# Kernel tuning notes

Hardware: AMD Instinct MI355X
Metric: run time of the kernel (lower is better)

Reference implementation:

```python
import jax, jax.numpy as jnp
import numpy as np

B, D, H, E, K, A = 65536, 44, 256, 4, 2, 8  # batch, state_dim, hidden, experts, top_k, action_dim


def setup_inputs() -> dict:
    key = jax.random.key(0)
    ks = jax.random.split(key, 10)
    s = 0.1  # weight scale
    return dict(
        state=jax.random.normal(ks[0], (B, D), dtype=jnp.float32),
        rW1=jax.random.normal(ks[1], (D, H // 2)) * s, rb1=jnp.zeros((H // 2,)),
        rW2=jax.random.normal(ks[2], (H // 2, E)) * s, rb2=jnp.zeros((E,)),
        eW1=jax.random.normal(ks[3], (E, D, H)) * s, eb1=jnp.zeros((E, H)),
        eg1=jnp.ones((E, H)), ebt1=jnp.zeros((E, H)),
        eW2=jax.random.normal(ks[4], (E, H, H)) * s, eb2=jnp.zeros((E, H)),
        eg2=jnp.ones((E, H)), ebt2=jnp.zeros((E, H)),
        eW3=jax.random.normal(ks[5], (E, H, 2 * A)) * s, eb3=jnp.zeros((E, 2 * A)),
        vW1=jax.random.normal(ks[6], (D, H)) * s, vb1=jnp.zeros((H,)),
        vg=jnp.ones((H,)), vbt=jnp.zeros((H,)),
        vW2=jax.random.normal(ks[7], (H, H // 2)) * s, vb2=jnp.zeros((H // 2,)),
        vW3=jax.random.normal(ks[8], (H // 2, 1)) * s, vb3=jnp.zeros((1,)),
    )


def _ln(x, g, b):
    m = jnp.mean(x, axis=-1, keepdims=True)
    v = jnp.mean(jnp.square(x - m), axis=-1, keepdims=True)
    return (x - m) * jax.lax.rsqrt(v + 1e-5) * g + b


def reference(state, rW1, rb1, rW2, rb2,
              eW1, eb1, eg1, ebt1, eW2, eb2, eg2, ebt2, eW3, eb3,
              vW1, vb1, vg, vbt, vW2, vb2, vW3, vb3):
    # Router (eval mode: no noise)
    h = jax.nn.relu(state @ rW1 + rb1)
    router_probs = jax.nn.softmax(h @ rW2 + rb2, axis=-1)          # [B, E]
    top_v, top_i = jax.lax.top_k(router_probs, K)                  # [B, K]
    top_v = top_v / (jnp.sum(top_v, axis=-1, keepdims=True) + 1e-8)
    # Dense combine weights per expert (equivalent to per-sample gather/scatter loop)
    combine = jnp.sum(jax.nn.one_hot(top_i, E, dtype=state.dtype) * top_v[..., None], axis=1)  # [B, E]

    def expert(W1, b1, g1, bt1, W2, b2, g2, bt2, W3, b3):
        y = jax.nn.relu(_ln(state @ W1 + b1, g1, bt1))   # [B, H]
        y = jax.nn.relu(_ln(y @ W2 + b2, g2, bt2))       # [B, H]
        return y @ W3 + b3                               # [B, 2A]

    eout = jax.vmap(expert)(eW1, eb1, eg1, ebt1, eW2, eb2, eg2, ebt2, eW3, eb3)  # [E, B, 2A]
    mix = jnp.einsum('ebd,be->bd', eout, combine)        # [B, 2A]

    alpha = jax.nn.softplus(mix[:, :A]) + 1.0
    beta = jax.nn.softplus(mix[:, A:]) + 1.0

    v = jax.nn.relu(_ln(state @ vW1 + vb1, vg, vbt))
    v = jax.nn.relu(v @ vW2 + vb2)
    value = v @ vW3 + vb3                                # [B, 1]
    return alpha, beta, value, router_probs
```

## Files before the change

### kernel.cpp

```cpp
#include <hip/hip_runtime.h>
#include <math.h>

#define NB 65536

using f32x4 = __attribute__((ext_vector_type(4))) float;
using u32x4 = __attribute__((ext_vector_type(4))) unsigned;
using bf16x8 = __attribute__((ext_vector_type(8))) __bf16;

__device__ __forceinline__ unsigned pk2(float lo, float hi) {
    return (unsigned)__builtin_bit_cast(unsigned short, (__bf16)lo)
         | ((unsigned)__builtin_bit_cast(unsigned short, (__bf16)hi) << 16);
}
__device__ __forceinline__ float softplus_f(float x) {
    return fmaxf(x, 0.f) + log1pf(expf(-fabsf(x)));
}

#define MFMA16(acc, a, b) acc = __builtin_amdgcn_mfma_f32_16x16x32_bf16(a, b, acc, 0, 0, 0)

__device__ __forceinline__ bf16x8 cvt8(f32x4 a, f32x4 b) {
    union { bf16x8 v; unsigned u[4]; } r;
    r.u[0] = pk2(a[0], a[1]); r.u[1] = pk2(a[2], a[3]);
    r.u[2] = pk2(b[0], b[1]); r.u[3] = pk2(b[2], b[3]);
    return r.v;
}

__device__ __forceinline__ const bf16x8* ys_frag(const unsigned short* ys, int row, int col) {
    return (const bf16x8*)&ys[row * 256 + (col ^ ((row & 7) << 3))];
}

template<int NJ>
__device__ __forceinline__ void ldch(f32x4* r, const f32x4* __restrict__ src, int tid) {
    #pragma unroll
    for (int j = 0; j < NJ; ++j) r[j] = src[tid + j * 256];
}
template<int NJ>
__device__ __forceinline__ void wrch(unsigned short* buf, const f32x4* r, int tid) {
    #pragma unroll
    for (int j = 0; j < NJ; ++j) *(f32x4*)&buf[(size_t)(tid + j * 256) * 8] = r[j];
}

template<int NT>
__device__ __forceinline__ void mfma_bcols(f32x4* acc, bf16x8 a, const unsigned short* bufp, int c, int g) {
    #pragma unroll
    for (int t = 0; t < NT; ++t) {
        bf16x8 b = *(const bf16x8*)&bufp[t * 512 + g * 128 + c * 8];
        MFMA16(acc[t], a, b);
    }
}

__device__ __forceinline__ void ln_relu_store(
    f32x4* acc, const float* bs, const float* gs, const float* ts,
    unsigned int* ysu, int stripe, int g, int c)
{
    #pragma unroll
    for (int t = 0; t < 16; ++t) {
        float bb = bs[t * 16 + c];
        #pragma unroll
        for (int r = 0; r < 4; ++r) acc[t][r] += bb;
    }
    float sum[4] = {0.f, 0.f, 0.f, 0.f}, sq[4] = {0.f, 0.f, 0.f, 0.f};
    #pragma unroll
    for (int t = 0; t < 16; ++t) {
        #pragma unroll
        for (int r = 0; r < 4; ++r) { sum[r] += acc[t][r]; sq[r] += acc[t][r] * acc[t][r]; }
    }
    #pragma unroll
    for (int m = 1; m < 16; m <<= 1) {
        #pragma unroll
        for (int r = 0; r < 4; ++r) { sum[r] += __shfl_xor(sum[r], m); sq[r] += __shfl_xor(sq[r], m); }
    }
    float rs[4], nm[4];
    #pragma unroll
    for (int r = 0; r < 4; ++r) {
        float mean = sum[r] * (1.f / 256.f);
        float var = sq[r] * (1.f / 256.f) - mean * mean;
        rs[r] = rsqrtf(var + 1e-5f);
        nm[r] = -mean * rs[r];
    }
    const int odd = c & 1;
    const int ra = stripe + g * 4 + (odd ? 2 : 0);
    const int sza = (ra & 7) << 2, szb = ((ra + 1) & 7) << 2;
    #pragma unroll
    for (int t = 0; t < 16; ++t) {
        float gg = gs[t * 16 + c], bb = ts[t * 16 + c];
        float v0 = fmaxf(fmaf(fmaf(acc[t][0], rs[0], nm[0]), gg, bb), 0.f);
        float v1 = fmaxf(fmaf(fmaf(acc[t][1], rs[1], nm[1]), gg, bb), 0.f);
        float v2 = fmaxf(fmaf(fmaf(acc[t][2], rs[2], nm[2]), gg, bb), 0.f);
        float v3 = fmaxf(fmaf(fmaf(acc[t][3], rs[3], nm[3]), gg, bb), 0.f);
        float o0 = __shfl_xor(v0, 1), o1 = __shfl_xor(v1, 1);
        float o2 = __shfl_xor(v2, 1), o3 = __shfl_xor(v3, 1);
        unsigned p0 = pk2(odd ? o0 : v0, odd ? v0 : o0);
        unsigned p1 = pk2(odd ? o1 : v1, odd ? v1 : o1);
        unsigned p2 = pk2(odd ? o2 : v2, odd ? v2 : o2);
        unsigned p3 = pk2(odd ? o3 : v3, odd ? v3 : o3);
        unsigned pa = odd ? p2 : p0;
        unsigned pb = odd ? p3 : p1;
        int cp = t * 8 + (c >> 1);
        ysu[ra * 128 + (cp ^ sza)] = pa;
        ysu[(ra + 1) * 128 + (cp ^ szb)] = pb;
    }
}

__global__ __launch_bounds__(256) void k1_prep_router(
    const float* __restrict__ state,
    const float* __restrict__ rW1, const float* __restrict__ rb1,
    const float* __restrict__ rW2, const float* __restrict__ rb2,
    const float* __restrict__ eW1, const float* __restrict__ eW2, const float* __restrict__ eW3,
    const float* __restrict__ vW1, const float* __restrict__ vW2,
    unsigned int* __restrict__ w1img, unsigned int* __restrict__ w2img,
    unsigned int* __restrict__ vw1img, unsigned int* __restrict__ vw2img,
    unsigned int* __restrict__ w3img,
    float* __restrict__ out_probs, float* __restrict__ combine)
{
    __shared__ f32x4 pl[256];
    const int blk = blockIdx.x;
    if (blk < 192) {
        int fid = blk * 256 + threadIdx.x;
        float v[8];
        unsigned int* dst;
        if (fid < 8192) {
            int e = fid >> 11, ch = (fid >> 10) & 1, rr = fid & 1023;
            int t = rr >> 6, g = (rr >> 4) & 3, c = rr & 15;
            int h = t * 16 + c, k0 = ch * 32 + g * 8;
            #pragma unroll
            for (int j = 0; j < 8; ++j) {
                int k = k0 + j;
                v[j] = (k < 44) ? eW1[(e * 44 + k) * 256 + h] : 0.f;
            }
            dst = w1img + (size_t)fid * 4;
        } else if (fid < 40960) {
            int f = fid - 8192;
            int e = f >> 13, ch = (f >> 10) & 7, rr = f & 1023;
            int t = rr >> 6, g = (rr >> 4) & 3, c = rr & 15;
            int h = t * 16 + c, k0 = ch * 32 + g * 8;
            const float* base = eW2 + (size_t)e * 65536 + h;
            #pragma unroll
            for (int j = 0; j < 8; ++j) v[j] = base[(size_t)(k0 + j) * 256];
            dst = w2img + (size_t)f * 4;
        } else if (fid < 43008) {
            int f = fid - 40960;
            int ch = f >> 10, rr = f & 1023;
            int t = rr >> 6, g = (rr >> 4) & 3, c = rr & 15;
            int h = t * 16 + c, k0 = ch * 32 + g * 8;
            #pragma unroll
            for (int j = 0; j < 8; ++j) {
                int k = k0 + j;
                v[j] = (k < 44) ? vW1[k * 256 + h] : 0.f;
            }
            dst = vw1img + (size_t)f * 4;
        } else if (fid < 47104) {
            int f = fid - 43008;
            int ch = f >> 9, rr = f & 511;
            int t = rr >> 6, g = (rr >> 4) & 3, c = rr & 15;
            int h = t * 16 + c, k0 = ch * 32 + g * 8;
            #pragma unroll
            for (int j = 0; j < 8; ++j) v[j] = vW2[(k0 + j) * 128 + h];
            dst = vw2img + (size_t)f * 4;
        } else {
            int f = fid - 47104;
            int e = f >> 9, rr = f & 511;
            int s = rr >> 6, g = (rr >> 4) & 3, o = rr & 15;
            int k0 = s * 32 + g * 8;
            #pragma unroll
            for (int j = 0; j < 8; ++j) v[j] = eW3[(size_t)e * 4096 + (k0 + j) * 16 + o];
            dst = w3img + (size_t)f * 4;
        }
        u32x4 out;
        #pragma unroll
        for (int p = 0; p < 4; ++p) out[p] = pk2(v[2 * p], v[2 * p + 1]);
        *(u32x4*)dst = out;
        return;
    }

    const int tid = threadIdx.x;
    const int wid = tid >> 6;
    const int lane = tid & 63;
    const int brow = (blk - 192) * 64;
    const int w32 = __builtin_amdgcn_readfirstlane(wid * 32);

    {
        float s[44];
        const float* srow = state + (size_t)(brow + lane) * 44;
        #pragma unroll
        for (int d4 = 0; d4 < 11; ++d4) {
            f32x4 v = *(const f32x4*)(srow + d4 * 4);
            s[d4 * 4 + 0] = v[0]; s[d4 * 4 + 1] = v[1];
            s[d4 * 4 + 2] = v[2]; s[d4 * 4 + 3] = v[3];
        }
        const float* w1b = rW1 + w32;
        f32x4 h[8];
        #pragma unroll
        for (int j = 0; j < 8; ++j) h[j] = *(const f32x4*)&rb1[w32 + j * 4];
        #pragma unroll
        for (int d = 0; d < 44; ++d) {
            #pragma unroll
            for (int j = 0; j < 8; ++j)
                h[j] += s[d] * *(const f32x4*)(w1b + d * 128 + j * 4);
        }
        f32x4 l = {0.f, 0.f, 0.f, 0.f};
        #pragma unroll
        for (int j = 0; j < 8; ++j) {
            #pragma unroll
            for (int cmp = 0; cmp < 4; ++cmp) {
                float hv = fmaxf(h[j][cmp], 0.f);
                l += hv * *(const f32x4*)&rW2[(w32 + j * 4 + cmp) * 4];
            }
        }
        pl[wid * 64 + lane] = l;
    }
    __syncthreads();
    if (wid == 0) {
        f32x4 lg = pl[lane] + pl[64 + lane] + pl[128 + lane] + pl[192 + lane];
        lg += *(const f32x4*)rb2;
        float l0 = lg[0], l1 = lg[1], l2 = lg[2], l3 = lg[3];
        float mx = fmaxf(fmaxf(l0, l1), fmaxf(l2, l3));
        float e0 = expf(l0 - mx), e1 = expf(l1 - mx), e2 = expf(l2 - mx), e3 = expf(l3 - mx);
        float inv = 1.f / (e0 + e1 + e2 + e3);
        float p0 = e0 * inv, p1 = e1 * inv, p2 = e2 * inv, p3 = e3 * inv;
        f32x4 probs = {p0, p1, p2, p3};
        *(f32x4*)&out_probs[(size_t)(brow + lane) * 4] = probs;

        int i1 = 0; float v1 = p0;
        if (p1 > v1) { v1 = p1; i1 = 1; }
        if (p2 > v1) { v1 = p2; i1 = 2; }
        if (p3 > v1) { v1 = p3; i1 = 3; }
        int i2 = -1; float v2 = -1.f;
        if (i1 != 0 && p0 > v2) { v2 = p0; i2 = 0; }
        if (i1 != 1 && p1 > v2) { v2 = p1; i2 = 1; }
        if (i1 != 2 && p2 > v2) { v2 = p2; i2 = 2; }
        if (i1 != 3 && p3 > v2) { v2 = p3; i2 = 3; }
        float cn = 1.f / (v1 + v2 + 1e-8f);
        float c1 = v1 * cn, c2 = v2 * cn;
        f32x4 cm;
        cm[0] = (i1 == 0) ? c1 : (i2 == 0) ? c2 : 0.f;
        cm[1] = (i1 == 1) ? c1 : (i2 == 1) ? c2 : 0.f;
        cm[2] = (i1 == 2) ? c1 : (i2 == 2) ? c2 : 0.f;
        cm[3] = (i1 == 3) ? c1 : (i2 == 3) ? c2 : 0.f;
        *(f32x4*)&combine[(size_t)(brow + lane) * 4] = cm;
    }
}

#define SM_YS    0
#define SM_BUFA  32768
#define SM_BUFB  49152
#define SM_B1    65536
#define SM_G1    66560
#define SM_T1    67584
#define SM_B2    68608
#define SM_G2    69632
#define SM_T2    70656
#define SM_B3    71680
#define SM_CMB   71744
#define SM_TOTAL 72768

#define SWAPBUF() { unsigned short* _t = cur; cur = nxt; nxt = _t; }

__global__ __launch_bounds__(256, 2) void k2_experts_value(
    const float* __restrict__ state,
    const float* __restrict__ eb1, const float* __restrict__ eg1, const float* __restrict__ ebt1,
    const float* __restrict__ eb2, const float* __restrict__ eg2, const float* __restrict__ ebt2,
    const float* __restrict__ eb3,
    const float* __restrict__ vb1, const float* __restrict__ vg, const float* __restrict__ vbt,
    const float* __restrict__ vb2, const float* __restrict__ vW3, const float* __restrict__ vb3,
    const f32x4* __restrict__ w1v, const f32x4* __restrict__ w2v,
    const f32x4* __restrict__ vw1v, const f32x4* __restrict__ vw2v,
    const f32x4* __restrict__ w3v,
    const float* __restrict__ combine,
    float* __restrict__ out_alpha, float* __restrict__ out_beta, float* __restrict__ out_value)
{
    __shared__ __align__(16) unsigned char smem[SM_TOTAL];
    unsigned short* ys = (unsigned short*)(smem + SM_YS);
    unsigned int* ysu = (unsigned int*)(smem + SM_YS);
    float* b1s = (float*)(smem + SM_B1);
    float* g1s = (float*)(smem + SM_G1);
    float* t1s = (float*)(smem + SM_T1);
    float* b2s = (float*)(smem + SM_B2);
    float* g2s = (float*)(smem + SM_G2);
    float* t2s = (float*)(smem + SM_T2);
    float* b3s = (float*)(smem + SM_B3);
    float* cmbs = (float*)(smem + SM_CMB);
    unsigned short* cur = (unsigned short*)(smem + SM_BUFA);
    unsigned short* nxt = (unsigned short*)(smem + SM_BUFB);

    const int tid = threadIdx.x;
    const int wid = tid >> 6;
    const int lane = tid & 63;
    const int c = lane & 15;
    const int g = lane >> 4;
    const int stripe = wid * 16;
    const bool is_expert = (blockIdx.x < 1024);
    const int brow = (is_expert ? blockIdx.x : (blockIdx.x - 1024)) * 64;

    bf16x8 a1[2];
    {
        const float* srow = state + (size_t)(brow + stripe + c) * 44;
        f32x4 v0 = *(const f32x4*)(srow + g * 8);
        f32x4 v1 = *(const f32x4*)(srow + g * 8 + 4);
        a1[0] = cvt8(v0, v1);
        f32x4 z = {0.f, 0.f, 0.f, 0.f};
        f32x4 w0 = z, w1 = z;
        if (g == 0) { w0 = *(const f32x4*)(srow + 32); w1 = *(const f32x4*)(srow + 36); }
        else if (g == 1) { w0 = *(const f32x4*)(srow + 40); }
        a1[1] = cvt8(w0, w1);
    }

    f32x4 r[4];

    if (is_expert) {
        cmbs[tid] = combine[(size_t)brow * 4 + tid];
        float mix0 = 0.f, mix1 = 0.f, mix2 = 0.f, mix3 = 0.f;

        ldch<4>(r, w1v, tid);
        wrch<4>(cur, r, tid);
        ldch<4>(r, w1v + 1024, tid);
        __syncthreads();

        for (int e = 0; e < 4; ++e) {
            const int en = (e < 3) ? e + 1 : 3;
            float xb1 = eb1[e * 256 + tid], xg1 = eg1[e * 256 + tid], xt1 = ebt1[e * 256 + tid];
            float xb2 = eb2[e * 256 + tid], xg2 = eg2[e * 256 + tid], xt2 = ebt2[e * 256 + tid];
            b1s[tid] = xb1; g1s[tid] = xg1; t1s[tid] = xt1;
            b2s[tid] = xb2; g2s[tid] = xg2; t2s[tid] = xt2;
            if (tid < 16) b3s[tid] = eb3[e * 16 + tid];

            f32x4 acc1[16];
            #pragma unroll
            for (int t = 0; t < 16; ++t) acc1[t] = (f32x4){0.f, 0.f, 0.f, 0.f};

            wrch<4>(nxt, r, tid);
            ldch<4>(r, w2v + (size_t)(e * 8 + 0) * 1024, tid);
            mfma_bcols<16>(acc1, a1[0], cur, c, g);
            __syncthreads(); SWAPBUF();

            wrch<4>(nxt, r, tid);
            ldch<4>(r, w2v + (size_t)(e * 8 + 1) * 1024, tid);
            mfma_bcols<16>(acc1, a1[1], cur, c, g);
            ln_relu_store(acc1, b1s, g1s, t1s, ysu, stripe, g, c);
            __syncthreads(); SWAPBUF();

            f32x4 acc2[16];
            #pragma unroll
            for (int t = 0; t < 16; ++t) acc2[t] = (f32x4){0.f, 0.f, 0.f, 0.f};

            #pragma unroll
            for (int ch = 0; ch < 7; ++ch) {
                wrch<4>(nxt, r, tid);
                if (ch < 6) ldch<4>(r, w2v + (size_t)(e * 8 + ch + 2) * 1024, tid);
                else        ldch<2>(r, w3v + (size_t)e * 512, tid);
                bf16x8 a = *ys_frag(ys, stripe + c, ch * 32 + g * 8);
                mfma_bcols<16>(acc2, a, cur, c, g);
                __syncthreads(); SWAPBUF();
            }

            wrch<2>(nxt, r, tid);
            ldch<4>(r, w1v + (size_t)(en * 2) * 1024, tid);
            {
                bf16x8 a = *ys_frag(ys, stripe + c, 7 * 32 + g * 8);
                mfma_bcols<16>(acc2, a, cur, c, g);
            }
            ln_relu_store(acc2, b2s, g2s, t2s, ysu, stripe, g, c);
            __syncthreads(); SWAPBUF();

            wrch<4>(nxt, r, tid);
            ldch<4>(r, w1v + (size_t)(en * 2 + 1) * 1024, tid);
            f32x4 acc3 = (f32x4){0.f, 0.f, 0.f, 0.f};
            #pragma unroll
            for (int s = 0; s < 8; ++s) {
                bf16x8 a = *ys_frag(ys, stripe + c, s * 32 + g * 8);
                bf16x8 b = *(const bf16x8*)&cur[s * 512 + g * 128 + c * 8];
                MFMA16(acc3, a, b);
            }
            float bb3 = b3s[c];
            mix0 += cmbs[(stripe + g * 4 + 0) * 4 + e] * (acc3[0] + bb3);
            mix1 += cmbs[(stripe + g * 4 + 1) * 4 + e] * (acc3[1] + bb3);
            mix2 += cmbs[(stripe + g * 4 + 2) * 4 + e] * (acc3[2] + bb3);
            mix3 += cmbs[(stripe + g * 4 + 3) * 4 + e] * (acc3[3] + bb3);
            __syncthreads(); SWAPBUF();
        }

        int row0 = brow + stripe + g * 4;
        float sp0 = softplus_f(mix0) + 1.f;
        float sp1 = softplus_f(mix1) + 1.f;
        float sp2 = softplus_f(mix2) + 1.f;
        float sp3 = softplus_f(mix3) + 1.f;
        if (c < 8) {
            out_alpha[(size_t)(row0 + 0) * 8 + c] = sp0;
            out_alpha[(size_t)(row0 + 1) * 8 + c] = sp1;
            out_alpha[(size_t)(row0 + 2) * 8 + c] = sp2;
            out_alpha[(size_t)(row0 + 3) * 8 + c] = sp3;
        } else {
            out_beta[(size_t)(row0 + 0) * 8 + (c - 8)] = sp0;
            out_beta[(size_t)(row0 + 1) * 8 + (c - 8)] = sp1;
            out_beta[(size_t)(row0 + 2) * 8 + (c - 8)] = sp2;
            out_beta[(size_t)(row0 + 3) * 8 + (c - 8)] = sp3;
        }
    } else {
        b1s[tid] = vb1[tid]; g1s[tid] = vg[tid]; t1s[tid] = vbt[tid];
        if (tid < 128) { b2s[tid] = vb2[tid]; g2s[tid] = vW3[tid]; }

        ldch<4>(r, vw1v, tid);
        wrch<4>(cur, r, tid);
        ldch<4>(r, vw1v + 1024, tid);
        __syncthreads();

        f32x4 acc1[16];
        #pragma unroll
        for (int t = 0; t < 16; ++t) acc1[t] = (f32x4){0.f, 0.f, 0.f, 0.f};

        wrch<4>(nxt, r, tid);
        ldch<2>(r, vw2v, tid);
        mfma_bcols<16>(acc1, a1[0], cur, c, g);
        __syncthreads(); SWAPBUF();

        wrch<4>(nxt, r, tid);
        ldch<2>(r, vw2v + 512, tid);
        mfma_bcols<16>(acc1, a1[1], cur, c, g);
        ln_relu_store(acc1, b1s, g1s, t1s, ysu, stripe, g, c);
        __syncthreads(); SWAPBUF();

        f32x4 acc2[8];
        #pragma unroll
        for (int t = 0; t < 8; ++t) acc2[t] = (f32x4){0.f, 0.f, 0.f, 0.f};

        #pragma unroll
        for (int ch = 0; ch < 7; ++ch) {
            wrch<2>(nxt, r, tid);
            if (ch < 6) ldch<2>(r, vw2v + (size_t)(ch + 2) * 512, tid);
            bf16x8 a = *ys_frag(ys, stripe + c, ch * 32 + g * 8);
            mfma_bcols<8>(acc2, a, cur, c, g);
            __syncthreads(); SWAPBUF();
        }
        {
            bf16x8 a = *ys_frag(ys, stripe + c, 7 * 32 + g * 8);
            mfma_bcols<8>(acc2, a, cur, c, g);
        }

        float part[4] = {0.f, 0.f, 0.f, 0.f};
        #pragma unroll
        for (int t = 0; t < 8; ++t) {
            float bb = b2s[t * 16 + c], ww = g2s[t * 16 + c];
            #pragma unroll
            for (int q = 0; q < 4; ++q) part[q] += fmaxf(acc2[t][q] + bb, 0.f) * ww;
        }
        #pragma unroll
        for (int m = 1; m < 16; m <<= 1) {
            #pragma unroll
            for (int q = 0; q < 4; ++q) part[q] += __shfl_xor(part[q], m);
        }
        if (c == 0) {
            float v3 = vb3[0];
            int row = brow + stripe + g * 4;
            out_value[row + 0] = part[0] + v3;
            out_value[row + 1] = part[1] + v3;
            out_value[row + 2] = part[2] + v3;
            out_value[row + 3] = part[3] + v3;
        }
    }
}

extern "C" void kernel_launch(void* const* d_in, const int* in_sizes, int n_in,
                              void* d_out, int out_size, void* d_ws, size_t ws_size,
                              hipStream_t stream)
{
    const float* state = (const float*)d_in[0];
    const float* rW1  = (const float*)d_in[1];
    const float* rb1  = (const float*)d_in[2];
    const float* rW2  = (const float*)d_in[3];
    const float* rb2  = (const float*)d_in[4];
    const float* eW1  = (const float*)d_in[5];
    const float* eb1  = (const float*)d_in[6];
    const float* eg1  = (const float*)d_in[7];
    const float* ebt1 = (const float*)d_in[8];
    const float* eW2  = (const float*)d_in[9];
    const float* eb2  = (const float*)d_in[10];
    const float* eg2  = (const float*)d_in[11];
    const float* ebt2 = (const float*)d_in[12];
    const float* eW3  = (const float*)d_in[13];
    const float* eb3  = (const float*)d_in[14];
    const float* vW1  = (const float*)d_in[15];
    const float* vb1  = (const float*)d_in[16];
    const float* vg   = (const float*)d_in[17];
    const float* vbt  = (const float*)d_in[18];
    const float* vW2  = (const float*)d_in[19];
    const float* vb2  = (const float*)d_in[20];
    const float* vW3  = (const float*)d_in[21];
    const float* vb3  = (const float*)d_in[22];

    float* out = (float*)d_out;
    float* out_alpha = out;
    float* out_beta  = out + (size_t)NB * 8;
    float* out_value = out + (size_t)NB * 16;
    float* out_probs = out + (size_t)NB * 17;

    char* ws = (char*)d_ws;
    float* combine        = (float*)ws;
    unsigned int* w1img   = (unsigned int*)(ws + 0x100000);
    unsigned int* w2img   = (unsigned int*)(ws + 0x120000);
    unsigned int* vw1img  = (unsigned int*)(ws + 0x1A0000);
    unsigned int* vw2img  = (unsigned int*)(ws + 0x1A8000);
    unsigned int* w3img   = (unsigned int*)(ws + 0x1B8000);

    hipLaunchKernelGGL(k1_prep_router, dim3(1216), dim3(256), 0, stream,
                       state, rW1, rb1, rW2, rb2, eW1, eW2, eW3, vW1, vW2,
                       w1img, w2img, vw1img, vw2img, w3img, out_probs, combine);
    hipLaunchKernelGGL(k2_experts_value, dim3(2048), dim3(256), 0, stream,
                       state, eb1, eg1, ebt1, eb2, eg2, ebt2, eb3,
                       vb1, vg, vbt, vb2, vW3, vb3,
                       (const f32x4*)w1img, (const f32x4*)w2img,
                       (const f32x4*)vw1img, (const f32x4*)vw2img,
                       (const f32x4*)w3img,
                       combine, out_alpha, out_beta, out_value);
}
```

Before: 259.2 us.

## Stage router state in LDS with 2 rows per thread; use non-draining barriers

```diff
diff --git a/kernel.cpp b/kernel.cpp
--- a/kernel.cpp
+++ b/kernel.cpp
@@ -13,6 +13,12 @@
 }
 __device__ __forceinline__ float softplus_f(float x) {
     return fmaxf(x, 0.f) + log1pf(expf(-fabsf(x)));
+}
+
+__device__ __forceinline__ void barrier_nodrain() {
+    asm volatile("s_waitcnt lgkmcnt(0)" ::: "memory");
+    __builtin_amdgcn_s_barrier();
+    __builtin_amdgcn_sched_barrier(0);
 }
 
 #define MFMA16(acc, a, b) acc = __builtin_amdgcn_mfma_f32_16x16x32_bf16(a, b, acc, 0, 0, 0)
@@ -112,7 +118,7 @@
     unsigned int* __restrict__ w3img,
     float* __restrict__ out_probs, float* __restrict__ combine)
 {
-    __shared__ f32x4 pl[256];
+    __shared__ __align__(16) float rsm[44 * 128 + 4 * 128 * 4];
     const int blk = blockIdx.x;
     if (blk < 192) {
         int fid = blk * 256 + threadIdx.x;
@@ -175,42 +181,59 @@
     const int tid = threadIdx.x;
     const int wid = tid >> 6;
     const int lane = tid & 63;
-    const int brow = (blk - 192) * 64;
+    const int brow = (blk - 192) * 128;
+    float* s_lds = rsm;
+    f32x4* pl = (f32x4*)(rsm + 44 * 128);
+
+    {
+        int i = tid & 127, half = tid >> 7;
+        const float* srow = state + (size_t)(brow + i) * 44;
+        int d40 = half ? 6 : 0, d41 = half ? 11 : 6;
+        for (int d4 = d40; d4 < d41; ++d4) {
+            f32x4 v = *(const f32x4*)(srow + d4 * 4);
+            #pragma unroll
+            for (int q = 0; q < 4; ++q) {
+                int d = d4 * 4 + q;
+                if (d < 44) s_lds[d * 128 + i] = v[q];
+            }
+        }
+    }
+    __syncthreads();
+
     const int w32 = __builtin_amdgcn_readfirstlane(wid * 32);
-
-    {
-        float s[44];
-        const float* srow = state + (size_t)(brow + lane) * 44;
-        #pragma unroll
-        for (int d4 = 0; d4 < 11; ++d4) {
-            f32x4 v = *(const f32x4*)(srow + d4 * 4);
-            s[d4 * 4 + 0] = v[0]; s[d4 * 4 + 1] = v[1];
-            s[d4 * 4 + 2] = v[2]; s[d4 * 4 + 3] = v[3];
-        }
-        const float* w1b = rW1 + w32;
-        f32x4 h[8];
-        #pragma unroll
-        for (int j = 0; j < 8; ++j) h[j] = *(const f32x4*)&rb1[w32 + j * 4];
-        #pragma unroll
-        for (int d = 0; d < 44; ++d) {
-            #pragma unroll
-            for (int j = 0; j < 8; ++j)
-                h[j] += s[d] * *(const f32x4*)(w1b + d * 128 + j * 4);
-        }
-        f32x4 l = {0.f, 0.f, 0.f, 0.f};
+    f32x4 h0[8], h1[8];
+    #pragma unroll
+    for (int j = 0; j < 8; ++j) {
+        f32x4 b = *(const f32x4*)&rb1[w32 + j * 4];
+        h0[j] = b; h1[j] = b;
+    }
+    for (int d = 0; d < 44; ++d) {
+        float sd0 = s_lds[d * 128 + lane];
+        float sd1 = s_lds[d * 128 + 64 + lane];
         #pragma unroll
         for (int j = 0; j < 8; ++j) {
-            #pragma unroll
-            for (int cmp = 0; cmp < 4; ++cmp) {
-                float hv = fmaxf(h[j][cmp], 0.f);
-                l += hv * *(const f32x4*)&rW2[(w32 + j * 4 + cmp) * 4];
-            }
-        }
-        pl[wid * 64 + lane] = l;
-    }
+            f32x4 w = *(const f32x4*)(rW1 + d * 128 + w32 + j * 4);
+            h0[j] += sd0 * w;
+            h1[j] += sd1 * w;
+        }
+    }
+    f32x4 l0v = {0.f, 0.f, 0.f, 0.f}, l1v = {0.f, 0.f, 0.f, 0.f};
+    #pragma unroll
+    for (int j = 0; j < 8; ++j) {
+        #pragma unroll
+        for (int q = 0; q < 4; ++q) {
+            f32x4 w2 = *(const f32x4*)&rW2[(w32 + j * 4 + q) * 4];
+            l0v += fmaxf(h0[j][q], 0.f) * w2;
+            l1v += fmaxf(h1[j][q], 0.f) * w2;
+        }
+    }
+    pl[wid * 128 + lane] = l0v;
+    pl[wid * 128 + 64 + lane] = l1v;
     __syncthreads();
-    if (wid == 0) {
-        f32x4 lg = pl[lane] + pl[64 + lane] + pl[128 + lane] + pl[192 + lane];
+
+    if (wid < 2) {
+        int s = wid * 64 + lane;
+        f32x4 lg = pl[s] + pl[128 + s] + pl[256 + s] + pl[384 + s];
         lg += *(const f32x4*)rb2;
         float l0 = lg[0], l1 = lg[1], l2 = lg[2], l3 = lg[3];
         float mx = fmaxf(fmaxf(l0, l1), fmaxf(l2, l3));
@@ -218,7 +241,7 @@
         float inv = 1.f / (e0 + e1 + e2 + e3);
         float p0 = e0 * inv, p1 = e1 * inv, p2 = e2 * inv, p3 = e3 * inv;
         f32x4 probs = {p0, p1, p2, p3};
-        *(f32x4*)&out_probs[(size_t)(brow + lane) * 4] = probs;
+        *(f32x4*)&out_probs[(size_t)(brow + s) * 4] = probs;
 
         int i1 = 0; float v1 = p0;
         if (p1 > v1) { v1 = p1; i1 = 1; }
@@ -236,7 +259,7 @@
         cm[1] = (i1 == 1) ? c1 : (i2 == 1) ? c2 : 0.f;
         cm[2] = (i1 == 2) ? c1 : (i2 == 2) ? c2 : 0.f;
         cm[3] = (i1 == 3) ? c1 : (i2 == 3) ? c2 : 0.f;
-        *(f32x4*)&combine[(size_t)(brow + lane) * 4] = cm;
+        *(f32x4*)&combine[(size_t)(brow + s) * 4] = cm;
     }
 }
 
@@ -313,7 +336,7 @@
         ldch<4>(r, w1v, tid);
         wrch<4>(cur, r, tid);
         ldch<4>(r, w1v + 1024, tid);
-        __syncthreads();
+        barrier_nodrain();
 
         for (int e = 0; e < 4; ++e) {
             const int en = (e < 3) ? e + 1 : 3;
@@ -330,13 +353,13 @@
             wrch<4>(nxt, r, tid);
             ldch<4>(r, w2v + (size_t)(e * 8 + 0) * 1024, tid);
             mfma_bcols<16>(acc1, a1[0], cur, c, g);
-            __syncthreads(); SWAPBUF();
+            barrier_nodrain(); SWAPBUF();
 
             wrch<4>(nxt, r, tid);
             ldch<4>(r, w2v + (size_t)(e * 8 + 1) * 1024, tid);
             mfma_bcols<16>(acc1, a1[1], cur, c, g);
             ln_relu_store(acc1, b1s, g1s, t1s, ysu, stripe, g, c);
-            __syncthreads(); SWAPBUF();
+            barrier_nodrain(); SWAPBUF();
 
             f32x4 acc2[16];
             #pragma unroll
@@ -349,7 +372,7 @@
                 else        ldch<2>(r, w3v + (size_t)e * 512, tid);
                 bf16x8 a = *ys_frag(ys, stripe + c, ch * 32 + g * 8);
                 mfma_bcols<16>(acc2, a, cur, c, g);
-                __syncthreads(); SWAPBUF();
+                barrier_nodrain(); SWAPBUF();
             }
 
             wrch<2>(nxt, r, tid);
@@ -359,7 +382,7 @@
                 mfma_bcols<16>(acc2, a, cur, c, g);
             }
             ln_relu_store(acc2, b2s, g2s, t2s, ysu, stripe, g, c);
-            __syncthreads(); SWAPBUF();
+            barrier_nodrain(); SWAPBUF();
 
             wrch<4>(nxt, r, tid);
             ldch<4>(r, w1v + (size_t)(en * 2 + 1) * 1024, tid);
@@ -375,7 +398,7 @@
             mix1 += cmbs[(stripe + g * 4 + 1) * 4 + e] * (acc3[1] + bb3);
             mix2 += cmbs[(stripe + g * 4 + 2) * 4 + e] * (acc3[2] + bb3);
             mix3 += cmbs[(stripe + g * 4 + 3) * 4 + e] * (acc3[3] + bb3);
-            __syncthreads(); SWAPBUF();
+            barrier_nodrain(); SWAPBUF();
         }
 
         int row0 = brow + stripe + g * 4;
@@ -401,7 +424,7 @@
         ldch<4>(r, vw1v, tid);
         wrch<4>(cur, r, tid);
         ldch<4>(r, vw1v + 1024, tid);
-        __syncthreads();
+        barrier_nodrain();
 
         f32x4 acc1[16];
         #pragma unroll
@@ -410,13 +433,13 @@
         wrch<4>(nxt, r, tid);
         ldch<2>(r, vw2v, tid);
         mfma_bcols<16>(acc1, a1[0], cur, c, g);
-        __syncthreads(); SWAPBUF();
+        barrier_nodrain(); SWAPBUF();
 
         wrch<4>(nxt, r, tid);
         ldch<2>(r, vw2v + 512, tid);
         mfma_bcols<16>(acc1, a1[1], cur, c, g);
         ln_relu_store(acc1, b1s, g1s, t1s, ysu, stripe, g, c);
-        __syncthreads(); SWAPBUF();
+        barrier_nodrain(); SWAPBUF();
 
         f32x4 acc2[8];
         #pragma unroll
@@ -428,7 +451,7 @@
             if (ch < 6) ldch<2>(r, vw2v + (size_t)(ch + 2) * 512, tid);
             bf16x8 a = *ys_frag(ys, stripe + c, ch * 32 + g * 8);
             mfma_bcols<8>(acc2, a, cur, c, g);
-            __syncthreads(); SWAPBUF();
+            barrier_nodrain(); SWAPBUF();
         }
         {
             bf16x8 a = *ys_frag(ys, stripe + c, 7 * 32 + g * 8);
@@ -500,7 +523,7 @@
     unsigned int* vw2img  = (unsigned int*)(ws + 0x1A8000);
     unsigned int* w3img   = (unsigned int*)(ws + 0x1B8000);
 
-    hipLaunchKernelGGL(k1_prep_router, dim3(1216), dim3(256), 0, stream,
+    hipLaunchKernelGGL(k1_prep_router, dim3(704), dim3(256), 0, stream,
                        state, rW1, rb1, rW2, rb2, eW1, eW2, eW3, vW1, vW2,
                        w1img, w2img, vw1img, vw2img, w3img, out_probs, combine);
     hipLaunchKernelGGL(k2_experts_value, dim3(2048), dim3(256), 0, stream,
```

Result: no change. 261.1 us (+0.7%).
